# Kernel optimization log

Hardware: AMD Instinct MI355X
Metric: run time of the kernel (lower is better)

## Reference

```python
import jax, jax.numpy as jnp
import numpy as np


def setup_inputs() -> dict:
    key = jax.random.key(0)
    k1, k2 = jax.random.split(key)
    src = jax.random.normal(k1, (4096, 1024, 3), dtype=jnp.float32)
    tgt = jax.random.normal(k2, (4096, 1024, 3), dtype=jnp.float32)
    return {"src": src, "tgt": tgt}


def reference(src, tgt):
    # src, tgt: [bs, N, 3] -> work in [bs, 3, N] like the torch module
    src_t = jnp.swapaxes(src, 1, 2)                      # [bs, 3, N]
    tgt_t = jnp.swapaxes(tgt, 1, 2)                      # [bs, 3, N]
    src_mean = src_t.mean(axis=2, keepdims=True)         # [bs, 3, 1]
    tgt_mean = tgt_t.mean(axis=2, keepdims=True)         # [bs, 3, 1]
    src_c = src_t - src_mean                             # [bs, 3, N]
    tgt_c = tgt_t - tgt_mean                             # [bs, 3, N]
    # Cross-covariance H = src_c @ tgt_c^T : [bs, 3, 3]
    H = jnp.einsum('bin,bjn->bij', src_c, tgt_c)
    u, s, vh = jnp.linalg.svd(H)                         # H = u diag(s) vh
    v = jnp.swapaxes(vh, 1, 2)                           # torch.svd's v
    ut = jnp.swapaxes(u, 1, 2)
    R0 = jnp.matmul(v, ut)                               # candidate rotation
    det = jnp.linalg.det(R0)                             # [bs]
    # If det < 0, multiply v by reflect=diag(1,1,-1), i.e. negate last column of v
    sign = jnp.where(det < 0, -1.0, 1.0).astype(src.dtype)  # [bs]
    col_scale = jnp.stack(
        [jnp.ones_like(sign), jnp.ones_like(sign), sign], axis=-1
    )[:, None, :]                                        # [bs, 1, 3]
    R = jnp.matmul(v * col_scale, ut)                    # [bs, 3, 3]
    t = (-jnp.matmul(R, src_mean) + tgt_mean)[..., 0]    # [bs, 3]
    return (R, t)
```

## Files before the change

### kernel.cpp

```cpp
#include <hip/hip_runtime.h>
#include <math.h>

constexpr int NPTS = 1024;
constexpr int WPB = 4;

struct F3 { float x, y, z; };

__global__ __launch_bounds__(256, 4) void reduce_kernel(
    const float* __restrict__ src, const float* __restrict__ tgt,
    float* __restrict__ ws, int nbatch)
{
    const int wave = threadIdx.x >> 6;
    const int lane = threadIdx.x & 63;
    const int b = blockIdx.x * WPB + wave;
    if (b >= nbatch) return;

    const size_t base = (size_t)b * (NPTS * 3);
    const F3* __restrict__ ps = (const F3*)(src + base);
    const F3* __restrict__ pt = (const F3*)(tgt + base);

    float acc[15];
#pragma unroll
    for (int i = 0; i < 15; ++i) acc[i] = 0.f;

#pragma unroll
    for (int k = 0; k < 16; ++k) {
        const int p = k * 64 + lane;
        F3 s = ps[p];
        F3 t = pt[p];
        acc[0] += s.x; acc[1] += s.y; acc[2] += s.z;
        acc[3] += t.x; acc[4] += t.y; acc[5] += t.z;
        acc[6]  += s.x * t.x; acc[7]  += s.x * t.y; acc[8]  += s.x * t.z;
        acc[9]  += s.y * t.x; acc[10] += s.y * t.y; acc[11] += s.y * t.z;
        acc[12] += s.z * t.x; acc[13] += s.z * t.y; acc[14] += s.z * t.z;
    }

#pragma unroll
    for (int off = 32; off >= 1; off >>= 1) {
#pragma unroll
        for (int i = 0; i < 15; ++i)
            acc[i] += __shfl_down(acc[i], off, 64);
    }

    if (lane == 0) {
        float4* w = (float4*)(ws + (size_t)b * 16);
        w[0] = make_float4(acc[0],  acc[1],  acc[2],  acc[3]);
        w[1] = make_float4(acc[4],  acc[5],  acc[6],  acc[7]);
        w[2] = make_float4(acc[8],  acc[9],  acc[10], acc[11]);
        w[3] = make_float4(acc[12], acc[13], acc[14], 0.f);
    }
}

__device__ __forceinline__ float frcp(float x)  { return __builtin_amdgcn_rcpf(x); }
__device__ __forceinline__ float frsq(float x)  { return __builtin_amdgcn_rsqf(x); }
__device__ __forceinline__ float fsqrt(float x) { return __builtin_amdgcn_sqrtf(x); }

__global__ __launch_bounds__(256) void svd_kernel(
    const float* __restrict__ ws, float* __restrict__ out, int nbatch)
{
    const int b = blockIdx.x * 256 + threadIdx.x;
    if (b >= nbatch) return;

    const float4* w = (const float4*)(ws + (size_t)b * 16);
    float4 w0 = w[0], w1 = w[1], w2 = w[2], w3 = w[3];
    float r[15] = {w0.x, w0.y, w0.z, w0.w,
                   w1.x, w1.y, w1.z, w1.w,
                   w2.x, w2.y, w2.z, w2.w,
                   w3.x, w3.y, w3.z};

    const float invN = 1.0f / (float)NPTS;
    float mus[3] = {r[0] * invN, r[1] * invN, r[2] * invN};
    float mut[3] = {r[3] * invN, r[4] * invN, r[5] * invN};

    float H[3][3];
#pragma unroll
    for (int i = 0; i < 3; ++i)
#pragma unroll
        for (int j = 0; j < 3; ++j)
            H[i][j] = r[6 + i * 3 + j] - (float)NPTS * mus[i] * mut[j];

    float A[3][3];
#pragma unroll
    for (int i = 0; i < 3; ++i)
#pragma unroll
        for (int j = 0; j < 3; ++j)
            A[i][j] = H[0][i] * H[0][j] + H[1][i] * H[1][j] + H[2][i] * H[2][j];

    float V[3][3] = {{1.f, 0.f, 0.f}, {0.f, 1.f, 0.f}, {0.f, 0.f, 1.f}};
    auto rot = [&](int p, int q) {
        float apq = A[p][q];
        float diff = A[q][q] - A[p][p];
        float theta = diff * frcp(2.0f * apq);
        float t = copysignf(frcp(fabsf(theta) + fsqrt(fmaf(theta, theta, 1.0f))), theta);
        t = (fabsf(apq) < 1e-20f) ? 0.0f : t;
        float c = frsq(fmaf(t, t, 1.0f));
        float s = t * c;
#pragma unroll
        for (int k = 0; k < 3; ++k) {
            float akp = A[k][p], akq = A[k][q];
            A[k][p] = c * akp - s * akq;
            A[k][q] = s * akp + c * akq;
        }
#pragma unroll
        for (int k = 0; k < 3; ++k) {
            float apk = A[p][k], aqk = A[q][k];
            A[p][k] = c * apk - s * aqk;
            A[q][k] = s * apk + c * aqk;
        }
#pragma unroll
        for (int k = 0; k < 3; ++k) {
            float vkp = V[k][p], vkq = V[k][q];
            V[k][p] = c * vkp - s * vkq;
            V[k][q] = s * vkp + c * vkq;
        }
    };
#pragma unroll
    for (int sweep = 0; sweep < 4; ++sweep) {
        rot(0, 1);
        rot(0, 2);
        rot(1, 2);
    }

    float l0 = A[0][0], l1 = A[1][1], l2 = A[2][2];
    float e0[3] = {V[0][0], V[1][0], V[2][0]};
    float e1[3] = {V[0][1], V[1][1], V[2][1]};
    float e2[3] = {V[0][2], V[1][2], V[2][2]};
    auto cswap = [](float& la, float* va, float& lb, float* vb) {
        bool sw = lb > la;
        float tl = sw ? lb : la;
        lb = sw ? la : lb;
        la = tl;
#pragma unroll
        for (int k = 0; k < 3; ++k) {
            float tv2 = sw ? vb[k] : va[k];
            vb[k] = sw ? va[k] : vb[k];
            va[k] = tv2;
        }
    };
    cswap(l0, e0, l1, e1);
    cswap(l0, e0, l2, e2);
    cswap(l1, e1, l2, e2);

    float *v1 = e0, *v2 = e1, *v3 = e2;

    float u1[3], u2[3], u3[3], hv[3];
    hv[0] = H[0][0]*v1[0] + H[0][1]*v1[1] + H[0][2]*v1[2];
    hv[1] = H[1][0]*v1[0] + H[1][1]*v1[1] + H[1][2]*v1[2];
    hv[2] = H[2][0]*v1[0] + H[2][1]*v1[1] + H[2][2]*v1[2];
    {
        float n = frsq(fmaf(hv[0], hv[0], fmaf(hv[1], hv[1], hv[2]*hv[2])) + 1e-30f);
        u1[0] = hv[0] * n; u1[1] = hv[1] * n; u1[2] = hv[2] * n;
    }
    hv[0] = H[0][0]*v2[0] + H[0][1]*v2[1] + H[0][2]*v2[2];
    hv[1] = H[1][0]*v2[0] + H[1][1]*v2[1] + H[1][2]*v2[2];
    hv[2] = H[2][0]*v2[0] + H[2][1]*v2[1] + H[2][2]*v2[2];
    {
        float d = u1[0]*hv[0] + u1[1]*hv[1] + u1[2]*hv[2];
        hv[0] -= d * u1[0]; hv[1] -= d * u1[1]; hv[2] -= d * u1[2];
        float n = frsq(fmaf(hv[0], hv[0], fmaf(hv[1], hv[1], hv[2]*hv[2])) + 1e-30f);
        u2[0] = hv[0] * n; u2[1] = hv[1] * n; u2[2] = hv[2] * n;
    }
    u3[0] = u1[1]*u2[2] - u1[2]*u2[1];
    u3[1] = u1[2]*u2[0] - u1[0]*u2[2];
    u3[2] = u1[0]*u2[1] - u1[1]*u2[0];

    float cx = v1[1]*v2[2] - v1[2]*v2[1];
    float cy = v1[2]*v2[0] - v1[0]*v2[2];
    float cz = v1[0]*v2[1] - v1[1]*v2[0];
    float detV = cx * v3[0] + cy * v3[1] + cz * v3[2];
    float d3 = (detV < 0.f) ? -1.f : 1.f;

    float R[3][3];
#pragma unroll
    for (int i = 0; i < 3; ++i)
#pragma unroll
        for (int j = 0; j < 3; ++j)
            R[i][j] = v1[i]*u1[j] + v2[i]*u2[j] + d3 * v3[i]*u3[j];

    float tvec[3];
#pragma unroll
    for (int i = 0; i < 3; ++i)
        tvec[i] = mut[i] - (R[i][0]*mus[0] + R[i][1]*mus[1] + R[i][2]*mus[2]);

    float* Rout = out + (size_t)b * 9;
#pragma unroll
    for (int i = 0; i < 3; ++i)
#pragma unroll
        for (int j = 0; j < 3; ++j)
            Rout[i * 3 + j] = R[i][j];
    float* tout = out + (size_t)nbatch * 9 + (size_t)b * 3;
#pragma unroll
    for (int i = 0; i < 3; ++i) tout[i] = tvec[i];
}

extern "C" void kernel_launch(void* const* d_in, const int* in_sizes, int n_in,
                              void* d_out, int out_size, void* d_ws, size_t ws_size,
                              hipStream_t stream) {
    const float* src = (const float*)d_in[0];
    const float* tgt = (const float*)d_in[1];
    float* out = (float*)d_out;
    float* ws = (float*)d_ws;
    const int nbatch = in_sizes[0] / (NPTS * 3);

    const int nblocksA = (nbatch + WPB - 1) / WPB;
    reduce_kernel<<<nblocksA, 256, 0, stream>>>(src, tgt, ws, nbatch);

    const int nblocksB = (nbatch + 255) / 256;
    svd_kernel<<<nblocksB, 256, 0, stream>>>(ws, out, nbatch);
}
```

Baseline: 24.39 us.

## Fuse reduction and SVD solve into a single kernel via shared memory

Merges the per-batch moment reduction and the 3x3 SVD/rotation solve into one kernel. Each wave reduces one batch, writes its 15 sums to shared memory, and after a block barrier four lanes of wave 0 each solve one batch's SVD. This removes the second launch and the workspace write/read round trip. In exchange, the SVD runs on only four lanes per block, adds a barrier, and may raise register pressure in the streaming kernel.

```diff
diff --git a/kernel.cpp b/kernel.cpp
--- a/kernel.cpp
+++ b/kernel.cpp
@@ -5,69 +5,15 @@
 constexpr int WPB = 4;
 
 struct F3 { float x, y, z; };
-
-__global__ __launch_bounds__(256, 4) void reduce_kernel(
-    const float* __restrict__ src, const float* __restrict__ tgt,
-    float* __restrict__ ws, int nbatch)
-{
-    const int wave = threadIdx.x >> 6;
-    const int lane = threadIdx.x & 63;
-    const int b = blockIdx.x * WPB + wave;
-    if (b >= nbatch) return;
-
-    const size_t base = (size_t)b * (NPTS * 3);
-    const F3* __restrict__ ps = (const F3*)(src + base);
-    const F3* __restrict__ pt = (const F3*)(tgt + base);
-
-    float acc[15];
-#pragma unroll
-    for (int i = 0; i < 15; ++i) acc[i] = 0.f;
-
-#pragma unroll
-    for (int k = 0; k < 16; ++k) {
-        const int p = k * 64 + lane;
-        F3 s = ps[p];
-        F3 t = pt[p];
-        acc[0] += s.x; acc[1] += s.y; acc[2] += s.z;
-        acc[3] += t.x; acc[4] += t.y; acc[5] += t.z;
-        acc[6]  += s.x * t.x; acc[7]  += s.x * t.y; acc[8]  += s.x * t.z;
-        acc[9]  += s.y * t.x; acc[10] += s.y * t.y; acc[11] += s.y * t.z;
-        acc[12] += s.z * t.x; acc[13] += s.z * t.y; acc[14] += s.z * t.z;
-    }
-
-#pragma unroll
-    for (int off = 32; off >= 1; off >>= 1) {
-#pragma unroll
-        for (int i = 0; i < 15; ++i)
-            acc[i] += __shfl_down(acc[i], off, 64);
-    }
-
-    if (lane == 0) {
-        float4* w = (float4*)(ws + (size_t)b * 16);
-        w[0] = make_float4(acc[0],  acc[1],  acc[2],  acc[3]);
-        w[1] = make_float4(acc[4],  acc[5],  acc[6],  acc[7]);
-        w[2] = make_float4(acc[8],  acc[9],  acc[10], acc[11]);
-        w[3] = make_float4(acc[12], acc[13], acc[14], 0.f);
-    }
-}
 
 __device__ __forceinline__ float frcp(float x)  { return __builtin_amdgcn_rcpf(x); }
 __device__ __forceinline__ float frsq(float x)  { return __builtin_amdgcn_rsqf(x); }
 __device__ __forceinline__ float fsqrt(float x) { return __builtin_amdgcn_sqrtf(x); }
 
-__global__ __launch_bounds__(256) void svd_kernel(
-    const float* __restrict__ ws, float* __restrict__ out, int nbatch)
+__device__ __forceinline__ void svd_solve(const float* __restrict__ r,
+                                          float* __restrict__ out,
+                                          int b, int nbatch)
 {
-    const int b = blockIdx.x * 256 + threadIdx.x;
-    if (b >= nbatch) return;
-
-    const float4* w = (const float4*)(ws + (size_t)b * 16);
-    float4 w0 = w[0], w1 = w[1], w2 = w[2], w3 = w[3];
-    float r[15] = {w0.x, w0.y, w0.z, w0.w,
-                   w1.x, w1.y, w1.z, w1.w,
-                   w2.x, w2.y, w2.z, w2.w,
-                   w3.x, w3.y, w3.z};
-
     const float invN = 1.0f / (float)NPTS;
     float mus[3] = {r[0] * invN, r[1] * invN, r[2] * invN};
     float mut[3] = {r[3] * invN, r[4] * invN, r[5] * invN};
@@ -193,18 +139,68 @@
     for (int i = 0; i < 3; ++i) tout[i] = tvec[i];
 }
 
+__global__ __launch_bounds__(256, 4) void kabsch_fused(
+    const float* __restrict__ src, const float* __restrict__ tgt,
+    float* __restrict__ out, int nbatch)
+{
+    const int wave = threadIdx.x >> 6;
+    const int lane = threadIdx.x & 63;
+    const int b = blockIdx.x * WPB + wave;
+
+    float acc[15];
+#pragma unroll
+    for (int i = 0; i < 15; ++i) acc[i] = 0.f;
+
+    if (b < nbatch) {
+        const size_t base = (size_t)b * (NPTS * 3);
+        const F3* __restrict__ ps = (const F3*)(src + base);
+        const F3* __restrict__ pt = (const F3*)(tgt + base);
+#pragma unroll
+        for (int k = 0; k < 16; ++k) {
+            const int p = k * 64 + lane;
+            F3 s = ps[p];
+            F3 t = pt[p];
+            acc[0] += s.x; acc[1] += s.y; acc[2] += s.z;
+            acc[3] += t.x; acc[4] += t.y; acc[5] += t.z;
+            acc[6]  += s.x * t.x; acc[7]  += s.x * t.y; acc[8]  += s.x * t.z;
+            acc[9]  += s.y * t.x; acc[10] += s.y * t.y; acc[11] += s.y * t.z;
+            acc[12] += s.z * t.x; acc[13] += s.z * t.y; acc[14] += s.z * t.z;
+        }
+    }
+
+#pragma unroll
+    for (int off = 32; off >= 1; off >>= 1) {
+#pragma unroll
+        for (int i = 0; i < 15; ++i)
+            acc[i] += __shfl_down(acc[i], off, 64);
+    }
+
+    __shared__ float smem[WPB][16];
+    if (b < nbatch && lane == 0) {
+#pragma unroll
+        for (int i = 0; i < 15; ++i) smem[wave][i] = acc[i];
+    }
+    __syncthreads();
+
+    if (wave == 0 && lane < WPB) {
+        const int sb = blockIdx.x * WPB + lane;
+        if (sb < nbatch) {
+            float r[15];
+#pragma unroll
+            for (int i = 0; i < 15; ++i) r[i] = smem[lane][i];
+            svd_solve(r, out, sb, nbatch);
+        }
+    }
+}
+
 extern "C" void kernel_launch(void* const* d_in, const int* in_sizes, int n_in,
                               void* d_out, int out_size, void* d_ws, size_t ws_size,
                               hipStream_t stream) {
     const float* src = (const float*)d_in[0];
     const float* tgt = (const float*)d_in[1];
     float* out = (float*)d_out;
-    float* ws = (float*)d_ws;
     const int nbatch = in_sizes[0] / (NPTS * 3);
 
-    const int nblocksA = (nbatch + WPB - 1) / WPB;
-    reduce_kernel<<<nblocksA, 256, 0, stream>>>(src, tgt, ws, nbatch);
-
-    const int nblocksB = (nbatch + 255) / 256;
-    svd_kernel<<<nblocksB, 256, 0, stream>>>(ws, out, nbatch);
+    const int nblocks = (nbatch + WPB - 1) / WPB;
+    kabsch_fused<<<nblocks, 256, 0, stream>>>(src, tgt, out, nbatch);
 }
```

Result: slower. 25.53 us (+4.7%).
